# Kernel optimization log

Hardware: AMD Instinct MI355X
Metric: run time of the kernel (lower is better)

Reference implementation:

```python
import jax, jax.numpy as jnp
import numpy as np

HIDDEN = 1024
HEADS = 16
HEAD_DIM = HIDDEN // HEADS  # 64
B, S = 4, 2048


def setup_inputs() -> dict:
    key = jax.random.key(0)
    ks = jax.random.split(key, 9)
    sd = 1.0 / np.sqrt(HIDDEN)
    return {
        "hidden_state": jax.random.normal(ks[0], (B, S, HIDDEN), dtype=jnp.float32),
        "Wq": jax.random.uniform(ks[1], (HIDDEN, HIDDEN), jnp.float32, -sd, sd),
        "bq": jax.random.uniform(ks[2], (HIDDEN,), jnp.float32, -sd, sd),
        "Wk": jax.random.uniform(ks[3], (HIDDEN, HEAD_DIM), jnp.float32, -sd, sd),
        "bk": jax.random.uniform(ks[4], (HEAD_DIM,), jnp.float32, -sd, sd),
        "Wv": jax.random.uniform(ks[5], (HIDDEN, HEAD_DIM), jnp.float32, -sd, sd),
        "bv": jax.random.uniform(ks[6], (HEAD_DIM,), jnp.float32, -sd, sd),
        "Wo": jax.random.uniform(ks[7], (HIDDEN, HIDDEN), jnp.float32, -sd, sd),
        "bo": jax.random.uniform(ks[8], (HIDDEN,), jnp.float32, -sd, sd),
    }


def reference(hidden_state, Wq, bq, Wk, bk, Wv, bv, Wo, bo):
    b, s, _ = hidden_state.shape
    # projections
    q = hidden_state @ Wq + bq               # [B,S,H*Dh]
    k = hidden_state @ Wk + bk               # [B,S,Dh] (shared across heads)
    v = hidden_state @ Wv + bv               # [B,S,Dh]
    q = q.reshape(b, s, HEADS, HEAD_DIM)     # [B,S,H,Dh]
    scale = 1.0 / jnp.sqrt(jnp.float32(HEAD_DIM))
    # scores: [B,H,S,S] — shared K broadcast over heads via einsum
    scores = jnp.einsum("bqhd,bkd->bhqk", q, k) * scale
    probs = jax.nn.softmax(scores, axis=-1)
    out = jnp.einsum("bhqk,bkd->bqhd", probs, v)  # [B,S,H,Dh]
    out = out.reshape(b, s, HEADS * HEAD_DIM)
    return out @ Wo + bo
```

## Files before the change

kernel.cpp:

```cpp
#include <hip/hip_runtime.h>
#include <hip/hip_bf16.h>
#include <cstdint>

#define HIDDEN 1024
#define HEADS 16
#define HEAD_DIM 64
#define BB 4
#define SS 2048
#define NTOK (BB * SS)

typedef __attribute__((ext_vector_type(8))) __bf16 bf16x8;
typedef __attribute__((ext_vector_type(4))) float f32x4;
typedef unsigned short u16;

#define PSCALE 0.1803368801111137f

__device__ __forceinline__ u16 f2bf(float x) {
    union { float f; uint32_t u; } v; v.f = x;
    uint32_t r = v.u + 0x7FFF + ((v.u >> 16) & 1);
    return (u16)(r >> 16);
}

typedef __attribute__((address_space(3))) uint32_t lds_u32;
typedef __attribute__((address_space(1))) uint32_t glb_u32;
__device__ __forceinline__ void gload16(const u16* g, u16* l) {
    __builtin_amdgcn_global_load_lds((const glb_u32*)g, (lds_u32*)l, 16, 0, 0);
}

__global__ void cvt_f32_bf16(const float* __restrict__ in, u16* __restrict__ out, int n4) {
    int i = blockIdx.x * blockDim.x + threadIdx.x;
    int stride = gridDim.x * blockDim.x;
    for (; i < n4; i += stride) {
        float4 v = ((const float4*)in)[i];
        ushort4 o;
        o.x = f2bf(v.x); o.y = f2bf(v.y); o.z = f2bf(v.z); o.w = f2bf(v.w);
        ((ushort4*)out)[i] = o;
    }
}

__global__ void transpose4_to_bf16(const float* __restrict__ Wq, const float* __restrict__ Wk,
                                   const float* __restrict__ Wv, const float* __restrict__ Wo,
                                   u16* __restrict__ Wta, u16* __restrict__ Wot) {
    __shared__ float tile[32][33];
    const int z = blockIdx.z;
    const int Nz = (z == 1 || z == 2) ? 64 : 1024;
    const int bx = blockIdx.x;
    if (bx * 32 >= Nz) return;
    const float* W = (z == 0) ? Wq : (z == 1) ? Wk : (z == 2) ? Wv : Wo;
    u16* Wt = (z == 0) ? Wta : (z == 1) ? (Wta + (size_t)1024 * HIDDEN)
              : (z == 2) ? (Wta + (size_t)1088 * HIDDEN) : Wot;
    const int by = blockIdx.y;
    const int tx = threadIdx.x;
    const int ty = threadIdx.y;
    for (int i = 0; i < 4; i++) {
        int kk = ty + i * 8;
        tile[kk][tx] = W[(size_t)(by * 32 + kk) * Nz + bx * 32 + tx];
    }
    __syncthreads();
    for (int i = 0; i < 4; i++) {
        int nn = ty + i * 8;
        Wt[(size_t)(bx * 32 + nn) * 1024 + by * 32 + tx] = f2bf(tile[tx][nn]);
    }
}


#define GEMM_PRE(APTR, BPTR)                                                         \
    __shared__ u16 Al[2][128 * 64];                                                  \
    __shared__ u16 Bl[2][128 * 64];                                                  \
    const int mb = blockIdx.y, nb = blockIdx.x;                                      \
    const int tid = threadIdx.x;                                                     \
    const int w = tid >> 6, lane = tid & 63;                                         \
    const int lr = lane & 15, lg = lane >> 4;                                        \
    const int wr = w >> 1, wc = w & 1;                                               \
    f32x4 acc[4][4] = {};                                                            \
    const int srow = lane >> 3;                                                      \
    const int scol = (lane & 7) * 8;                                                 \
    const u16* Ap = APTR + (size_t)(mb * 128 + w * 32 + srow) * 1024 + scol;         \
    const u16* Bp = BPTR + (size_t)(nb * 128 + w * 32 + srow) * 1024 + scol;

#define GSTAGE(BUF)                                                                  \
    do {                                                                             \
        _Pragma("unroll") for (int i = 0; i < 4; i++) {                              \
            gload16(Ap + (size_t)(i * 8) * 1024, &Al[BUF][(w * 32 + i * 8) * 64]);   \
            gload16(Bp + (size_t)(i * 8) * 1024, &Bl[BUF][(w * 32 + i * 8) * 64]);   \
        }                                                                            \
        Ap += 64;                                                                    \
        Bp += 64;                                                                    \
    } while (0)

#define GCOMPUTE(BUF)                                                                \
    do {                                                                             \
        _Pragma("unroll") for (int ks = 0; ks < 2; ks++) {                           \
            bf16x8 af[4], bfr[4];                                                    \
            _Pragma("unroll") for (int mf = 0; mf < 4; mf++)                         \
                af[mf] = *(const bf16x8*)(&Al[BUF][(wr * 64 + mf * 16 + lr) * 64 + ks * 32 + lg * 8]); \
            _Pragma("unroll") for (int nf = 0; nf < 4; nf++)                         \
                bfr[nf] = *(const bf16x8*)(&Bl[BUF][(wc * 64 + nf * 16 + lr) * 64 + ks * 32 + lg * 8]); \
            __builtin_amdgcn_s_setprio(1);                                           \
            _Pragma("unroll") for (int mf = 0; mf < 4; mf++)                         \
                _Pragma("unroll") for (int nf = 0; nf < 4; nf++)                     \
                    acc[mf][nf] = __builtin_amdgcn_mfma_f32_16x16x32_bf16(af[mf], bfr[nf], acc[mf][nf], 0, 0, 0); \
            __builtin_amdgcn_s_setprio(0);                                           \
        }                                                                            \
    } while (0)

#define GITER(BUF, DOSTAGE)                                        \
    do {                                                           \
        asm volatile("s_waitcnt vmcnt(0)" ::: "memory");           \
        __builtin_amdgcn_s_barrier();                              \
        if (DOSTAGE) GSTAGE(BUF ^ 1);                              \
        GCOMPUTE(BUF);                                             \
        asm volatile("" ::: "memory");                             \
    } while (0)

#define GEMM_LOOP()                                                \
    GSTAGE(0);                                                     \
    for (int i = 0; i < 7; i++) {                                  \
        GITER(0, 1);                                               \
        GITER(1, 1);                                               \
    }                                                              \
    GITER(0, 1);                                                   \
    GITER(1, 0);

__global__ __launch_bounds__(256) void gemm128_f32(
    const u16* __restrict__ A, const u16* __restrict__ Bt,
    const float* __restrict__ bias, float* __restrict__ C, int N) {
    GEMM_PRE(A, Bt);
    GEMM_LOOP();
#pragma unroll
    for (int nf = 0; nf < 4; nf++) {
        int n = nb * 128 + wc * 64 + nf * 16 + lr;
        float bval = bias[n];
#pragma unroll
        for (int mf = 0; mf < 4; mf++)
#pragma unroll
            for (int r = 0; r < 4; r++) {
                int m = mb * 128 + wr * 64 + mf * 16 + lg * 4 + r;
                C[(size_t)m * N + n] = acc[mf][nf][r] + bval;
            }
    }
}

#define NPROJ 1152
__global__ __launch_bounds__(256) void gemm_proj(
    const u16* __restrict__ A, const u16* __restrict__ Bt,
    const float* __restrict__ bq, const float* __restrict__ bk, const float* __restrict__ bv,
    u16* __restrict__ qout, u16* __restrict__ kout, u16* __restrict__ vout) {
    GEMM_PRE(A, Bt);
    GEMM_LOOP();
#pragma unroll
    for (int nf = 0; nf < 4; nf++) {
        int n = nb * 128 + wc * 64 + nf * 16 + lr;
        float bval = (n < 1024) ? bq[n] : (n < 1088) ? bk[n - 1024] : bv[n - 1088];
#pragma unroll
        for (int mf = 0; mf < 4; mf++)
#pragma unroll
            for (int r = 0; r < 4; r++) {
                int m = mb * 128 + wr * 64 + mf * 16 + lg * 4 + r;
                float val = acc[mf][nf][r] + bval;
                if (n < 1024) {
                    qout[(size_t)m * 1024 + n] = f2bf(val * PSCALE);
                } else if (n < 1088) {
                    kout[(size_t)m * 64 + (n - 1024)] = f2bf(val);
                } else {
                    int bb = m >> 11, t = m & (SS - 1);
                    vout[((size_t)bb * 64 + (n - 1088)) * SS + t] = f2bf(val);
                }
            }
    }
}

#define KVB 64
#define NT (SS / KVB)

__global__ __launch_bounds__(512) void attn_kernel(
    const u16* __restrict__ q,
    const u16* __restrict__ k,
    const u16* __restrict__ vt,
    u16* __restrict__ o) {
    const int qt = blockIdx.x, h = blockIdx.y, b = blockIdx.z;
    const int tid = threadIdx.x;
    const int w = tid >> 6, lane = tid & 63;
    const int lr = lane & 15, lg = lane >> 4;

    __shared__ u16 Kl[4][KVB * 64];
    __shared__ u16 Vl[4][KVB * 64];

    const u16* kbase = k + (size_t)b * SS * HEAD_DIM;
    const u16* vbase = vt + (size_t)b * HEAD_DIM * SS;
    const int rowbase = b * SS + qt * 256 + w * 32;

    const int srow = w * 8 + (lane >> 3);
    const int sc16 = (lane & 7) ^ (srow & 7);
    const u16* kp = kbase + (size_t)srow * HEAD_DIM + sc16 * 8;
    const u16* vp = vbase + (size_t)srow * SS + sc16 * 8;

    bf16x8 qf[2][2];
#pragma unroll
    for (int s = 0; s < 2; s++)
#pragma unroll
        for (int ks = 0; ks < 2; ks++)
            qf[s][ks] = *(const bf16x8*)(q + (size_t)(rowbase + s * 16 + lr) * HIDDEN + h * 64 + ks * 32 + lg * 8);

    bf16x8 onesf;
#pragma unroll
    for (int i = 0; i < 8; i++) onesf[i] = (__bf16)1.0f;

    const int xr = lr & 7;
    const int kvro0 = lr * 64 + ((lg) ^ xr) * 8;
    const int kvro1 = lr * 64 + ((4 + lg) ^ xr) * 8;

    f32x4 l_acc[2] = {};
    f32x4 oacc[2][4] = {};
    uint32_t pw[16];

#define VEXP(D, S) asm("v_exp_f32 %0, %1" : "=v"(D) : "v"(S))

#define STAGE(BUF)                            \
    do {                                      \
        gload16(kp, &Kl[BUF][w * 512]);       \
        gload16(vp, &Vl[BUF][w * 512]);       \
        kp += KVB * HEAD_DIM;                 \
        vp += KVB;                            \
    } while (0)

#define QKEXP(BUF)                                                                     \
    do {                                                                               \
        f32x4 st0[4] = {}, st1[4] = {};                                                \
        __builtin_amdgcn_s_setprio(1);                                                 \
        _Pragma("unroll") for (int nf = 0; nf < 4; nf++) {                             \
            bf16x8 kf = *(const bf16x8*)(&Kl[BUF][kvro0 + nf * 1024]);                 \
            st0[nf] = __builtin_amdgcn_mfma_f32_16x16x32_bf16(kf, qf[0][0], st0[nf], 0, 0, 0); \
            st1[nf] = __builtin_amdgcn_mfma_f32_16x16x32_bf16(kf, qf[1][0], st1[nf], 0, 0, 0); \
        }                                                                              \
        _Pragma("unroll") for (int nf = 0; nf < 4; nf++) {                             \
            bf16x8 kf = *(const bf16x8*)(&Kl[BUF][kvro1 + nf * 1024]);                 \
            st0[nf] = __builtin_amdgcn_mfma_f32_16x16x32_bf16(kf, qf[0][1], st0[nf], 0, 0, 0); \
            st1[nf] = __builtin_amdgcn_mfma_f32_16x16x32_bf16(kf, qf[1][1], st1[nf], 0, 0, 0); \
        }                                                                              \
        __builtin_amdgcn_s_setprio(0);                                                 \
        uint32_t c0[8], c1[8];                                                         \
        _Pragma("unroll") for (int nf = 0; nf < 4; nf++) {                             \
            float p0, p1, p2, p3, r0, r1, r2, r3;                                      \
            VEXP(p0, st0[nf][0]); VEXP(p1, st0[nf][1]);                                \
            VEXP(p2, st0[nf][2]); VEXP(p3, st0[nf][3]);                                \
            asm("v_cvt_pk_bf16_f32 %0, %1, %2" : "=v"(c0[nf * 2]) : "v"(p0), "v"(p1)); \
            asm("v_cvt_pk_bf16_f32 %0, %1, %2" : "=v"(c0[nf * 2 + 1]) : "v"(p2), "v"(p3)); \
            VEXP(r0, st1[nf][0]); VEXP(r1, st1[nf][1]);                                \
            VEXP(r2, st1[nf][2]); VEXP(r3, st1[nf][3]);                                \
            asm("v_cvt_pk_bf16_f32 %0, %1, %2" : "=v"(c1[nf * 2]) : "v"(r0), "v"(r1)); \
            asm("v_cvt_pk_bf16_f32 %0, %1, %2" : "=v"(c1[nf * 2 + 1]) : "v"(r2), "v"(r3)); \
        }                                                                              \
        _Pragma("unroll") for (int ks = 0; ks < 2; ks++) {                             \
            uint32_t u0 = c0[4 * ks], v0 = c0[4 * ks + 1], x0 = c0[4 * ks + 2], y0 = c0[4 * ks + 3]; \
            uint32_t u1 = c1[4 * ks], v1 = c1[4 * ks + 1], x1 = c1[4 * ks + 2], y1 = c1[4 * ks + 3]; \
            asm("v_permlane32_swap_b32 %0, %1" : "+v"(u0), "+v"(x0));                  \
            asm("v_permlane32_swap_b32 %0, %1" : "+v"(v0), "+v"(y0));                  \
            asm("v_permlane16_swap_b32 %0, %1" : "+v"(u0), "+v"(x0));                  \
            asm("v_permlane16_swap_b32 %0, %1" : "+v"(v0), "+v"(y0));                  \
            asm("v_permlane32_swap_b32 %0, %1" : "+v"(u1), "+v"(x1));                  \
            asm("v_permlane32_swap_b32 %0, %1" : "+v"(v1), "+v"(y1));                  \
            asm("v_permlane16_swap_b32 %0, %1" : "+v"(u1), "+v"(x1));                  \
            asm("v_permlane16_swap_b32 %0, %1" : "+v"(v1), "+v"(y1));                  \
            pw[ks * 4 + 0] = u0; pw[ks * 4 + 1] = v0;                                  \
            pw[ks * 4 + 2] = x0; pw[ks * 4 + 3] = y0;                                  \
            pw[8 + ks * 4 + 0] = u1; pw[8 + ks * 4 + 1] = v1;                          \
            pw[8 + ks * 4 + 2] = x1; pw[8 + ks * 4 + 3] = y1;                          \
        }                                                                              \
    } while (0)

#define PVACC(BUF)                                                                     \
    do {                                                                               \
        union { uint32_t wv[4]; bf16x8 v8; } pf0, pf1;                                 \
        __builtin_amdgcn_s_setprio(1);                                                 \
        _Pragma("unroll") for (int ks = 0; ks < 2; ks++) {                             \
            pf0.wv[0] = pw[ks * 4 + 0]; pf0.wv[1] = pw[ks * 4 + 1];                    \
            pf0.wv[2] = pw[ks * 4 + 2]; pf0.wv[3] = pw[ks * 4 + 3];                    \
            pf1.wv[0] = pw[8 + ks * 4 + 0]; pf1.wv[1] = pw[8 + ks * 4 + 1];            \
            pf1.wv[2] = pw[8 + ks * 4 + 2]; pf1.wv[3] = pw[8 + ks * 4 + 3];            \
            const int kvro = ks ? kvro1 : kvro0;                                       \
            l_acc[0] = __builtin_amdgcn_mfma_f32_16x16x32_bf16(pf0.v8, onesf, l_acc[0], 0, 0, 0); \
            l_acc[1] = __builtin_amdgcn_mfma_f32_16x16x32_bf16(pf1.v8, onesf, l_acc[1], 0, 0, 0); \
            _Pragma("unroll") for (int nf = 0; nf < 4; nf++) {                         \
                bf16x8 vf = *(const bf16x8*)(&Vl[BUF][kvro + nf * 1024]);              \
                oacc[0][nf] = __builtin_amdgcn_mfma_f32_16x16x32_bf16(pf0.v8, vf, oacc[0][nf], 0, 0, 0); \
                oacc[1][nf] = __builtin_amdgcn_mfma_f32_16x16x32_bf16(pf1.v8, vf, oacc[1][nf], 0, 0, 0); \
            }                                                                          \
        }                                                                              \
        __builtin_amdgcn_s_setprio(0);                                                 \
    } while (0)

#define ITER(BPV, BQK, BST, DOSTAGE, VM)                           \
    do {                                                           \
        asm volatile("s_waitcnt vmcnt(" #VM ")" ::: "memory");     \
        __builtin_amdgcn_s_barrier();                              \
        if (DOSTAGE) STAGE(BST);                                   \
        PVACC(BPV);                                                \
        QKEXP(BQK);                                                \
        asm volatile("" ::: "memory");                             \
    } while (0)

    STAGE(0);
    STAGE(1);
    asm volatile("s_waitcnt vmcnt(2)" ::: "memory");
    __builtin_amdgcn_s_barrier();
    STAGE(2);
    QKEXP(0);

    for (int i = 0; i < 7; i++) {
        ITER(0, 1, 3, 1, 2);
        ITER(1, 2, 0, 1, 2);
        ITER(2, 3, 1, 1, 2);
        ITER(3, 0, 2, 1, 2);
    }
    ITER(0, 1, 3, 1, 2);
    ITER(1, 2, 3, 0, 2);
    ITER(2, 3, 3, 0, 0);
    PVACC(3);

#undef ITER
#undef STAGE
#undef QKEXP
#undef PVACC
#undef VEXP

#pragma unroll
    for (int s = 0; s < 2; s++) {
        float li[4];
#pragma unroll
        for (int r = 0; r < 4; r++) li[r] = 1.0f / l_acc[s][r];
#pragma unroll
        for (int nf = 0; nf < 4; nf++)
#pragma unroll
            for (int r = 0; r < 4; r++) {
                float val = oacc[s][nf][r] * li[r];
                o[(size_t)(rowbase + s * 16 + lg * 4 + r) * HIDDEN + h * 64 + nf * 16 + lr] = f2bf(val);
            }
    }
}

extern "C" void kernel_launch(void* const* d_in, const int* in_sizes, int n_in,
                              void* d_out, int out_size, void* d_ws, size_t ws_size,
                              hipStream_t stream) {
    const float* h  = (const float*)d_in[0];
    const float* Wq = (const float*)d_in[1];
    const float* bq = (const float*)d_in[2];
    const float* Wk = (const float*)d_in[3];
    const float* bk = (const float*)d_in[4];
    const float* Wv = (const float*)d_in[5];
    const float* bv = (const float*)d_in[6];
    const float* Wo = (const float*)d_in[7];
    const float* bo = (const float*)d_in[8];

    char* ws = (char*)d_ws;
    u16* hbf  = (u16*)ws; ws += (size_t)NTOK * HIDDEN * 2;
    u16* Wta  = (u16*)ws; ws += (size_t)NPROJ * HIDDEN * 2;
    u16* Wot  = (u16*)ws; ws += (size_t)HIDDEN * HIDDEN * 2;
    u16* qbf  = (u16*)ws; ws += (size_t)NTOK * HIDDEN * 2;
    u16* kbf  = (u16*)ws; ws += (size_t)NTOK * HEAD_DIM * 2;
    u16* vtb  = (u16*)ws; ws += (size_t)NTOK * HEAD_DIM * 2;
    u16* obf  = (u16*)ws; ws += (size_t)NTOK * HIDDEN * 2;

    cvt_f32_bf16<<<2048, 256, 0, stream>>>(h, hbf, NTOK * HIDDEN / 4);
    transpose4_to_bf16<<<dim3(32, 32, 4), dim3(32, 8), 0, stream>>>(Wq, Wk, Wv, Wo, Wta, Wot);

    gemm_proj<<<dim3(NPROJ / 128, NTOK / 128), 256, 0, stream>>>(hbf, Wta, bq, bk, bv, qbf, kbf, vtb);

    attn_kernel<<<dim3(SS / 256, HEADS, BB), 512, 0, stream>>>(qbf, kbf, vtb, obf);

    gemm128_f32<<<dim3(HIDDEN / 128, NTOK / 128), 256, 0, stream>>>(obf, Wot, bo, (float*)d_out, HIDDEN);
}
```

Measured before the change: 155.0 us.

## Triple-buffer GEMM LDS pipeline and remap blocks across XCDs

Moves the two GEMM kernels from double to triple LDS buffering. The waitcnt now allows the newest stage's 8 loads to stay in flight while the oldest is consumed, so global loads overlap compute more deeply. The launch also changes to a 1-D grid with an XCD-aware block remap, so that consecutive tiles land on the same chiplet and L2 reuse improves. Shared memory rises from 64KB to 96KB per block, which may reduce occupancy.

```diff
diff --git a/kernel.cpp b/kernel.cpp
--- a/kernel.cpp
+++ b/kernel.cpp
@@ -64,10 +64,13 @@
 }
 
 
-#define GEMM_PRE(APTR, BPTR)                                                         \
-    __shared__ u16 Al[2][128 * 64];                                                  \
-    __shared__ u16 Bl[2][128 * 64];                                                  \
-    const int mb = blockIdx.y, nb = blockIdx.x;                                      \
+#define GEMM_PRE(APTR, BPTR, NWGN)                                                   \
+    __shared__ u16 Al[3][128 * 64];                                                  \
+    __shared__ u16 Bl[3][128 * 64];                                                  \
+    const int bid0 = blockIdx.x;                                                     \
+    const int chunk = gridDim.x >> 3;                                                \
+    const int nid = (bid0 & 7) * chunk + (bid0 >> 3);                                \
+    const int mb = nid / (NWGN), nb = nid % (NWGN);                                  \
     const int tid = threadIdx.x;                                                     \
     const int w = tid >> 6, lane = tid & 63;                                         \
     const int lr = lane & 15, lg = lane >> 4;                                        \
@@ -104,28 +107,32 @@
         }                                                                            \
     } while (0)
 
-#define GITER(BUF, DOSTAGE)                                        \
+#define GITER(BUF, DOSTAGE, STBUF, VM)                             \
     do {                                                           \
-        asm volatile("s_waitcnt vmcnt(0)" ::: "memory");           \
+        asm volatile("s_waitcnt vmcnt(" #VM ")" ::: "memory");     \
         __builtin_amdgcn_s_barrier();                              \
-        if (DOSTAGE) GSTAGE(BUF ^ 1);                              \
+        if (DOSTAGE) GSTAGE(STBUF);                                \
         GCOMPUTE(BUF);                                             \
         asm volatile("" ::: "memory");                             \
     } while (0)
 
 #define GEMM_LOOP()                                                \
     GSTAGE(0);                                                     \
-    for (int i = 0; i < 7; i++) {                                  \
-        GITER(0, 1);                                               \
-        GITER(1, 1);                                               \
+    GSTAGE(1);                                                     \
+    for (int i = 0; i < 4; i++) {                                  \
+        GITER(0, 1, 2, 8);                                         \
+        GITER(1, 1, 0, 8);                                         \
+        GITER(2, 1, 1, 8);                                         \
     }                                                              \
-    GITER(0, 1);                                                   \
-    GITER(1, 0);
+    GITER(0, 1, 2, 8);                                             \
+    GITER(1, 1, 0, 8);                                             \
+    GITER(2, 0, 0, 8);                                             \
+    GITER(0, 0, 0, 0);
 
 __global__ __launch_bounds__(256) void gemm128_f32(
     const u16* __restrict__ A, const u16* __restrict__ Bt,
-    const float* __restrict__ bias, float* __restrict__ C, int N) {
-    GEMM_PRE(A, Bt);
+    const float* __restrict__ bias, float* __restrict__ C) {
+    GEMM_PRE(A, Bt, 8);
     GEMM_LOOP();
 #pragma unroll
     for (int nf = 0; nf < 4; nf++) {
@@ -136,7 +143,7 @@
 #pragma unroll
             for (int r = 0; r < 4; r++) {
                 int m = mb * 128 + wr * 64 + mf * 16 + lg * 4 + r;
-                C[(size_t)m * N + n] = acc[mf][nf][r] + bval;
+                C[(size_t)m * 1024 + n] = acc[mf][nf][r] + bval;
             }
     }
 }
@@ -146,7 +153,7 @@
     const u16* __restrict__ A, const u16* __restrict__ Bt,
     const float* __restrict__ bq, const float* __restrict__ bk, const float* __restrict__ bv,
     u16* __restrict__ qout, u16* __restrict__ kout, u16* __restrict__ vout) {
-    GEMM_PRE(A, Bt);
+    GEMM_PRE(A, Bt, 9);
     GEMM_LOOP();
 #pragma unroll
     for (int nf = 0; nf < 4; nf++) {
@@ -364,9 +371,9 @@
     cvt_f32_bf16<<<2048, 256, 0, stream>>>(h, hbf, NTOK * HIDDEN / 4);
     transpose4_to_bf16<<<dim3(32, 32, 4), dim3(32, 8), 0, stream>>>(Wq, Wk, Wv, Wo, Wta, Wot);
 
-    gemm_proj<<<dim3(NPROJ / 128, NTOK / 128), 256, 0, stream>>>(hbf, Wta, bq, bk, bv, qbf, kbf, vtb);
+    gemm_proj<<<576, 256, 0, stream>>>(hbf, Wta, bq, bk, bv, qbf, kbf, vtb);
 
     attn_kernel<<<dim3(SS / 256, HEADS, BB), 512, 0, stream>>>(qbf, kbf, vtb, obf);
 
-    gemm128_f32<<<dim3(HIDDEN / 128, NTOK / 128), 256, 0, stream>>>(obf, Wot, bo, (float*)d_out, HIDDEN);
-}
+    gemm128_f32<<<512, 256, 0, stream>>>(obf, Wot, bo, (float*)d_out);
+}
```

Result: slower. 183.4 us (+18.3%).
